# Kernel tuning notes

Measured on AMD Instinct MI355X. Metric: run time of the kernel, lower is better.

## Reference

```python
import jax, jax.numpy as jnp
import numpy as np

B, NU, NI, D, P, C = 32768, 200000, 200000, 512, 8, 512
DC = D // P  # cluster_dim = 64
TAU = 1.0


def setup_inputs() -> dict:
    key = jax.random.key(0)
    k = jax.random.split(key, 6)
    return {
        "user_emb": jax.random.normal(k[0], (NU, D), jnp.float32),
        "centroids": jax.random.normal(k[1], (P, C, DC), jnp.float32),
        "item_mu": jax.random.normal(k[2], (NI, D), jnp.float32),
        "item_logvar": jax.random.normal(k[3], (NI, D), jnp.float32) * 0.1,
        "user_id": jax.random.randint(k[4], (B,), 0, NU, jnp.int64 if jax.config.jax_enable_x64 else jnp.int32),
        "item_id": jax.random.randint(k[5], (B,), 0, NI, jnp.int64 if jax.config.jax_enable_x64 else jnp.int32),
    }


def _encode_user(user_emb, centroids, user_id, key):
    # gather + split into P partitions: [B, P, DC]
    u = user_emb[user_id].reshape(-1, P, DC)
    # squared L2 distance via expansion (avoids [B,P,C,DC] intermediate)
    u2 = jnp.sum(u * u, axis=-1)                      # [B, P]
    c2 = jnp.sum(centroids * centroids, axis=-1)      # [P, C]
    cross = jnp.einsum("bpd,pcd->bpc", u, centroids)  # [B, P, C]
    dist2 = jnp.maximum(u2[:, :, None] + c2[None, :, :] - 2.0 * cross, 0.0)
    neg_dist = -jnp.sqrt(dist2 + 1e-12)               # logits = -pairwise L2
    logits = jax.nn.softmax(neg_dist, axis=-1)        # [B, P, C]
    # gumbel-softmax, hard=True (straight-through)
    gu = jax.random.uniform(key, neg_dist.shape, jnp.float32, 1e-10, 1.0)
    g = -jnp.log(-jnp.log(gu))
    y_soft = jax.nn.softmax((neg_dist + g) / TAU, axis=-1)
    onehot = jax.nn.one_hot(jnp.argmax(y_soft, axis=-1), C, dtype=y_soft.dtype)
    y_hard = onehot + y_soft - jax.lax.stop_gradient(y_soft)
    # gather selected centroid per partition and concat -> [B, D]
    enc = jnp.einsum("bpc,pcd->bpd", y_hard, centroids).reshape(-1, D)
    return enc, logits


def _reparameterize(mu, logvar, key):
    std = jnp.exp(0.5 * logvar)
    eps = jax.random.normal(key, std.shape, std.dtype)
    return eps * std + mu


def reference(user_emb, centroids, item_mu, item_logvar, user_id, item_id):
    key = jax.random.key(42)
    kg, ke = jax.random.split(key)
    user_vecs, logits = _encode_user(user_emb, centroids, user_id, kg)
    item_vecs = _reparameterize(item_mu[item_id], item_logvar[item_id], ke)
    score = jnp.sum(user_vecs * item_vecs, axis=-1)  # [B]
    return score, logits
```

## Files before the change

### kernel.cpp

```cpp
#include <hip/hip_runtime.h>
#include <cstdint>
#include <cstddef>

#define B_TOT 32768
#define NPART 8
#define NCLUS 512
#define DCL   64
#define DTOT  512
#define BTILE 16
#define ROWB  272

typedef _Float16 half8 __attribute__((ext_vector_type(8)));
typedef float    f32x4 __attribute__((ext_vector_type(4)));

__host__ __device__ __forceinline__ void tf2x32(uint32_t k0, uint32_t k1,
    uint32_t x0, uint32_t x1, uint32_t& o0, uint32_t& o1)
{
  const uint32_t k2 = k0 ^ k1 ^ 0x1BD11BDAu;
#define TFR(r) { x0 += x1; x1 = (x1 << r) | (x1 >> (32 - r)); x1 ^= x0; }
  x0 += k0; x1 += k1;
  TFR(13) TFR(15) TFR(26) TFR(6)
  x0 += k1; x1 += k2 + 1u;
  TFR(17) TFR(29) TFR(16) TFR(24)
  x0 += k2; x1 += k0 + 2u;
  TFR(13) TFR(15) TFR(26) TFR(6)
  x0 += k0; x1 += k1 + 3u;
  TFR(17) TFR(29) TFR(16) TFR(24)
  x0 += k1; x1 += k2 + 4u;
  TFR(13) TFR(15) TFR(26) TFR(6)
  x0 += k2; x1 += k0 + 5u;
#undef TFR
  o0 = x0; o1 = x1;
}

__device__ __forceinline__ uint32_t tf_bits32(uint32_t k0, uint32_t k1, uint32_t n)
{
  uint32_t a, b;
  tf2x32(k0, k1, 0u, n, a, b);
  return a ^ b;
}

__device__ __forceinline__ float erfinv_xla(float x)
{
  float w = -log1pf(-x * x);
  float p;
  if (w < 5.0f) {
    w = w - 2.5f;
    p = 2.81022636e-08f;
    p = fmaf(p, w, 3.43273939e-07f);
    p = fmaf(p, w, -3.5233877e-06f);
    p = fmaf(p, w, -4.39150654e-06f);
    p = fmaf(p, w, 0.00021858087f);
    p = fmaf(p, w, -0.00125372503f);
    p = fmaf(p, w, -0.00417768164f);
    p = fmaf(p, w, 0.246640727f);
    p = fmaf(p, w, 1.50140941f);
  } else {
    w = __builtin_amdgcn_sqrtf(w) - 3.0f;
    p = -0.000200214257f;
    p = fmaf(p, w, 0.000100950558f);
    p = fmaf(p, w, 0.00134934322f);
    p = fmaf(p, w, -0.00367342844f);
    p = fmaf(p, w, 0.00573950773f);
    p = fmaf(p, w, -0.0076224613f);
    p = fmaf(p, w, 0.00943887047f);
    p = fmaf(p, w, 1.00167406f);
    p = fmaf(p, w, 2.83297682f);
  }
  return p * x;
}

__global__ __launch_bounds__(256) void qvae_prep_kernel(
    const float* __restrict__ centroids, _Float16* __restrict__ cimg)
{
  const int idx = blockIdx.x * 256 + threadIdx.x;
  const float* row = centroids + (size_t)idx * DCL;
  _Float16* orow = (_Float16*)((char*)cimg + (size_t)idx * ROWB);
  float s = 0.f;
#pragma unroll
  for (int d = 0; d < DCL; d += 4) {
    const float4 v = *(const float4*)(row + d);
    s = fmaf(v.x, v.x, s);
    s = fmaf(v.y, v.y, s);
    s = fmaf(v.z, v.z, s);
    s = fmaf(v.w, v.w, s);
  }
  *(float*)(orow + 128) = s;
#pragma unroll
  for (int d = 0; d < DCL; d += 8) {
    const float4 v0 = *(const float4*)(row + d);
    const float4 v1 = *(const float4*)(row + d + 4);
    const float vv[8] = { v0.x, v0.y, v0.z, v0.w, v1.x, v1.y, v1.z, v1.w };
    half8 hh, ll;
#pragma unroll
    for (int j = 0; j < 8; ++j) {
      const _Float16 h = (_Float16)vv[j];
      hh[j] = h;
      ll[j] = (_Float16)(vv[j] - (float)h);
    }
    *(half8*)(orow + d) = hh;
    *(half8*)(orow + 64 + d) = ll;
  }
}

__global__ __launch_bounds__(256, 4) void qvae_main_kernel(
    const float* __restrict__ user_emb, const _Float16* __restrict__ cimg,
    const int* __restrict__ user_id, float* __restrict__ out_logits,
    int* __restrict__ sel, uint32_t kg0, uint32_t kg1)
{
  __shared__ float u2s[BTILE];
  __shared__ float zZ[4][BTILE];
  __shared__ float zS[4][BTILE];
  __shared__ int   zA[4][BTILE];

  const int p = blockIdx.y;
  const int bbase = blockIdx.x * BTILE;
  const int tid = threadIdx.x;
  const int w  = tid >> 6;
  const int l  = tid & 63;
  const int lr = l & 15;
  const int q  = l >> 4;

  const int uid = user_id[bbase + lr];
  const float* urow = user_emb + (size_t)uid * DTOT + p * DCL;
  float uf[16];
  {
    const float4 a0 = *(const float4*)(urow + q * 8);
    const float4 a1 = *(const float4*)(urow + q * 8 + 4);
    const float4 a2 = *(const float4*)(urow + 32 + q * 8);
    const float4 a3 = *(const float4*)(urow + 32 + q * 8 + 4);
    uf[0]=a0.x;  uf[1]=a0.y;  uf[2]=a0.z;  uf[3]=a0.w;
    uf[4]=a1.x;  uf[5]=a1.y;  uf[6]=a1.z;  uf[7]=a1.w;
    uf[8]=a2.x;  uf[9]=a2.y;  uf[10]=a2.z; uf[11]=a2.w;
    uf[12]=a3.x; uf[13]=a3.y; uf[14]=a3.z; uf[15]=a3.w;
  }
  half8 ah[2], al[2];
#pragma unroll
  for (int m = 0; m < 2; ++m)
#pragma unroll
    for (int j = 0; j < 8; ++j) {
      const float v = uf[m * 8 + j];
      const _Float16 h = (_Float16)v;
      ah[m][j] = h;
      al[m][j] = (_Float16)(v - (float)h);
    }
  {
    float s = 0.f;
#pragma unroll
    for (int i = 0; i < 16; ++i) s = fmaf(uf[i], uf[i], s);
    s += __shfl_xor(s, 16);
    s += __shfl_xor(s, 32);
    if (tid < BTILE) u2s[tid] = s;
  }
  __syncthreads();
  float u2r[4];
  {
    const float4 uv = *(const float4*)&u2s[q * 4];
    u2r[0]=uv.x; u2r[1]=uv.y; u2r[2]=uv.z; u2r[3]=uv.w;
  }

  const int wcol = w * 32 + lr;
  const uint32_t nbw =
      ((uint32_t)(bbase + q * 4) * 8u + (uint32_t)p) * 512u + (uint32_t)wcol;
  const char* cb = (const char*)cimg;
  const uint32_t rowoff =
      ((uint32_t)p * NCLUS + (uint32_t)wcol) * (uint32_t)ROWB + (uint32_t)q * 16u;

  float ereg[32];
  float Zs[4]  = { 0.f, 0.f, 0.f, 0.f };
  float smx[4] = { -3.4e38f, -3.4e38f, -3.4e38f, -3.4e38f };
  int   sag[4] = { 0, 0, 0, 0 };

#define CDELT(i) ((((i) >> 1) * 128) + (((i) & 1) * 16))
#define BDELT(i) ((uint32_t)(CDELT(i)) * (uint32_t)ROWB)

#define LOADT(S, i)                                                           \
  {                                                                           \
    const uint32_t vo = rowoff + BDELT(i);                                    \
    bh0##S = *(const half8*)(cb + vo);                                        \
    bh1##S = *(const half8*)(cb + vo + 64);                                   \
    bl0##S = *(const half8*)(cb + vo + 128);                                  \
    bl1##S = *(const half8*)(cb + vo + 192);                                  \
    c2##S  = *(const float*)(cb + (vo - q * 16) + 256);                       \
  }

#define COMPT(S, i)                                                           \
  {                                                                           \
    f32x4 acc = { 0.f, 0.f, 0.f, 0.f };                                       \
    acc = __builtin_amdgcn_mfma_f32_16x16x32_f16(ah[0], bh0##S, acc, 0, 0, 0);\
    acc = __builtin_amdgcn_mfma_f32_16x16x32_f16(ah[1], bh1##S, acc, 0, 0, 0);\
    acc = __builtin_amdgcn_mfma_f32_16x16x32_f16(al[0], bh0##S, acc, 0, 0, 0);\
    acc = __builtin_amdgcn_mfma_f32_16x16x32_f16(al[1], bh1##S, acc, 0, 0, 0);\
    acc = __builtin_amdgcn_mfma_f32_16x16x32_f16(ah[0], bl0##S, acc, 0, 0, 0);\
    acc = __builtin_amdgcn_mfma_f32_16x16x32_f16(ah[1], bl1##S, acc, 0, 0, 0);\
    const uint32_t ncol = nbw + (uint32_t)CDELT(i);                           \
    const int colc = wcol + CDELT(i);                                         \
    _Pragma("unroll")                                                         \
    for (int r = 0; r < 4; ++r) {                                             \
      const float u2c2 = __fadd_rn(u2r[r], c2##S);                            \
      const float d2 = fmaxf(fmaf(-2.0f, acc[r], u2c2), 0.0f);                \
      const float qd = __builtin_amdgcn_sqrtf(__fadd_rn(d2, 1e-12f));         \
      const uint32_t bits = tf_bits32(kg0, kg1, ncol + (uint32_t)r * 4096u);  \
      const float u01 = __uint_as_float((bits >> 9) | 0x3f800000u) - 1.0f;    \
      const float gu = __fadd_rn(u01, 1e-10f);   \
      const float g = -__logf(-__logf(gu));                                   \
      const float sc = __fsub_rn(g, qd);                                      \
      if (sc > smx[r]) { smx[r] = sc; sag[r] = colc; }                        \
      const float e = __expf(-qd);                   \
      ereg[(i) * 4 + r] = e;                                                  \
      Zs[r] = __fadd_rn(Zs[r], e);                                            \
    }                                                                         \
  }

  half8 bh0A, bh1A, bl0A, bl1A; float c2A;
  half8 bh0B, bh1B, bl0B, bl1B; float c2B;
  LOADT(A, 0)
  LOADT(B, 1)
  COMPT(A, 0)
  LOADT(A, 2)
  COMPT(B, 1)
  LOADT(B, 3)
  COMPT(A, 2)
  LOADT(A, 4)
  COMPT(B, 3)
  LOADT(B, 5)
  COMPT(A, 4)
  LOADT(A, 6)
  COMPT(B, 5)
  LOADT(B, 7)
  COMPT(A, 6)
  COMPT(B, 7)

#pragma unroll
  for (int m = 1; m < 16; m <<= 1) {
#pragma unroll
    for (int r = 0; r < 4; ++r) {
      Zs[r] += __shfl_xor(Zs[r], m);
      const float os = __shfl_xor(smx[r], m);
      const int   oa = __shfl_xor(sag[r], m);
      if (os > smx[r] || (os == smx[r] && oa < sag[r])) { smx[r] = os; sag[r] = oa; }
    }
  }
  if (lr == 0) {
#pragma unroll
    for (int r = 0; r < 4; ++r) {
      zZ[w][q * 4 + r] = Zs[r];
      zS[w][q * 4 + r] = smx[r];
      zA[w][q * 4 + r] = sag[r];
    }
  }
  __syncthreads();

  float Zf[4]  = { 0.f, 0.f, 0.f, 0.f };
  float smf[4] = { -3.4e38f, -3.4e38f, -3.4e38f, -3.4e38f };
  int   saf[4] = { 0, 0, 0, 0 };
#pragma unroll
  for (int wv = 0; wv < 4; ++wv) {
    const float4 zz = *(const float4*)&zZ[wv][q * 4];
    const float4 ss = *(const float4*)&zS[wv][q * 4];
    const int4   aa = *(const int4*)&zA[wv][q * 4];
    const float zv[4] = { zz.x, zz.y, zz.z, zz.w };
    const float sv[4] = { ss.x, ss.y, ss.z, ss.w };
    const int   av[4] = { aa.x, aa.y, aa.z, aa.w };
#pragma unroll
    for (int r = 0; r < 4; ++r) {
      Zf[r] = __fadd_rn(Zf[r], zv[r]);
      if (sv[r] > smf[r] || (sv[r] == smf[r] && av[r] < saf[r])) {
        smf[r] = sv[r]; saf[r] = av[r];
      }
    }
  }

  float inv[4];
#pragma unroll
  for (int r = 0; r < 4; ++r) inv[r] = __builtin_amdgcn_rcpf(Zf[r]);

  float* obase = out_logits + ((size_t)(bbase + q * 4) * 8 + p) * 512 + wcol;
#pragma unroll
  for (int i = 0; i < 8; ++i)
#pragma unroll
    for (int r = 0; r < 4; ++r)
      obase[(size_t)r * 4096 + CDELT(i)] = ereg[i * 4 + r] * inv[r];

  if (w == 0 && lr == 0) {
#pragma unroll
    for (int r = 0; r < 4; ++r)
      sel[(bbase + q * 4 + r) * NPART + p] = saf[r];
  }
#undef CDELT
#undef BDELT
#undef LOADT
#undef COMPT
}

__global__ __launch_bounds__(256) void qvae_score_kernel(
    const float* __restrict__ centroids, const float* __restrict__ item_mu,
    const float* __restrict__ item_logvar, const int* __restrict__ item_id,
    const int* __restrict__ sel, float* __restrict__ out_score,
    uint32_t ke0, uint32_t ke1)
{
  const int lane = threadIdx.x & 63;
  const int b = blockIdx.x * 4 + (threadIdx.x >> 6);
  const int iid = item_id[b];
  const int pp = lane >> 3;
  const int sc = sel[b * NPART + pp];

  const float* cen = centroids + ((size_t)pp * NCLUS + sc) * DCL + (lane & 7) * 8;
  const float* mu = item_mu + (size_t)iid * DTOT + lane * 8;
  const float* lv = item_logvar + (size_t)iid * DTOT + lane * 8;

  const float4 m0 = *(const float4*)mu;
  const float4 m1 = *(const float4*)(mu + 4);
  const float4 l0 = *(const float4*)lv;
  const float4 l1 = *(const float4*)(lv + 4);
  const float4 q0 = *(const float4*)cen;
  const float4 q1 = *(const float4*)(cen + 4);
  const float mua[8] = { m0.x, m0.y, m0.z, m0.w, m1.x, m1.y, m1.z, m1.w };
  const float lva[8] = { l0.x, l0.y, l0.z, l0.w, l1.x, l1.y, l1.z, l1.w };
  const float cna[8] = { q0.x, q0.y, q0.z, q0.w, q1.x, q1.y, q1.z, q1.w };

  const float LO = __int_as_float(0xBF7FFFFFu);
  const float SQ2 = __int_as_float(0x3FB504F3u);
  const uint32_t nb = (uint32_t)b * 512u + (uint32_t)lane * 8u;

  float acc = 0.f;
#pragma unroll
  for (int k = 0; k < 8; ++k) {
    const uint32_t bits = tf_bits32(ke0, ke1, nb + (uint32_t)k);
    const float u01 = __uint_as_float((bits >> 9) | 0x3f800000u) - 1.0f;
    const float uu = fmaxf(LO, __fadd_rn(__fmul_rn(u01, 2.0f), LO));
    const float eps = __fmul_rn(SQ2, erfinv_xla(uu));
    const float sd = __expf(__fmul_rn(0.5f, lva[k]));
    const float it = __fadd_rn(__fmul_rn(eps, sd), mua[k]);
    acc = fmaf(cna[k], it, acc);
  }
#pragma unroll
  for (int m = 1; m < 64; m <<= 1) acc += __shfl_xor(acc, m);
  if (lane == 0) out_score[b] = acc;
}

extern "C" void kernel_launch(void* const* d_in, const int* in_sizes, int n_in,
                              void* d_out, int out_size, void* d_ws, size_t ws_size,
                              hipStream_t stream)
{
  (void)in_sizes; (void)n_in; (void)out_size; (void)ws_size;

  const float* user_emb    = (const float*)d_in[0];
  const float* centroids   = (const float*)d_in[1];
  const float* item_mu     = (const float*)d_in[2];
  const float* item_logvar = (const float*)d_in[3];
  const int*   user_id     = (const int*)d_in[4];
  const int*   item_id     = (const int*)d_in[5];

  float* out_score  = (float*)d_out;
  float* out_logits = (float*)d_out + B_TOT;

  int*       sel  = (int*)d_ws;
  _Float16*  cimg = (_Float16*)((char*)d_ws + (size_t)B_TOT * NPART * 4);

  uint32_t kg0, kg1, ke0, ke1;
  tf2x32(0u, 42u, 0u, 0u, kg0, kg1);
  tf2x32(0u, 42u, 0u, 1u, ke0, ke1);

  qvae_prep_kernel<<<NPART * NCLUS / 256, 256, 0, stream>>>(centroids, cimg);

  dim3 g1(B_TOT / BTILE, NPART);
  qvae_main_kernel<<<g1, 256, 0, stream>>>(user_emb, cimg, user_id,
                                           out_logits, sel, kg0, kg1);
  qvae_score_kernel<<<B_TOT / 4, 256, 0, stream>>>(centroids, item_mu, item_logvar,
                                                   item_id, sel, out_score, ke0, ke1);
}
```

Baseline: 483.1 us.

## Replace gumbel argmax log with ratio comparison and split MFMA accumulators

The gumbel argmax is rewritten algebraically. Maximizing g - qd with g = -log(t) is the same as minimizing t / exp(-qd), so the second log per element is removed and the exp value already computed for the softmax is reused. The comparison is done by cross-multiplication, which avoids a division. The MFMA chain is split into two independent accumulators to shorten the dependency chain. Exact tie-breaking may change because of rounding, and the reductions now carry one extra value each.

```diff
diff --git a/kernel.cpp b/kernel.cpp
--- a/kernel.cpp
+++ b/kernel.cpp
@@ -110,7 +110,8 @@
 {
   __shared__ float u2s[BTILE];
   __shared__ float zZ[4][BTILE];
-  __shared__ float zS[4][BTILE];
+  __shared__ float zT[4][BTILE];
+  __shared__ float zE[4][BTILE];
   __shared__ int   zA[4][BTILE];
 
   const int p = blockIdx.y;
@@ -165,11 +166,13 @@
   const char* cb = (const char*)cimg;
   const uint32_t rowoff =
       ((uint32_t)p * NCLUS + (uint32_t)wcol) * (uint32_t)ROWB + (uint32_t)q * 16u;
+  const uint32_t c2off = rowoff - (uint32_t)(q * 16) + 256u;
 
   float ereg[32];
-  float Zs[4]  = { 0.f, 0.f, 0.f, 0.f };
-  float smx[4] = { -3.4e38f, -3.4e38f, -3.4e38f, -3.4e38f };
-  int   sag[4] = { 0, 0, 0, 0 };
+  float Zs[4] = { 0.f, 0.f, 0.f, 0.f };
+  float tmin[4] = { 3.4e38f, 3.4e38f, 3.4e38f, 3.4e38f };
+  float emin[4] = { 1.0f, 1.0f, 1.0f, 1.0f };
+  int   amin[4] = { 0, 0, 0, 0 };
 
 #define CDELT(i) ((((i) >> 1) * 128) + (((i) & 1) * 16))
 #define BDELT(i) ((uint32_t)(CDELT(i)) * (uint32_t)ROWB)
@@ -181,32 +184,35 @@
     bh1##S = *(const half8*)(cb + vo + 64);                                   \
     bl0##S = *(const half8*)(cb + vo + 128);                                  \
     bl1##S = *(const half8*)(cb + vo + 192);                                  \
-    c2##S  = *(const float*)(cb + (vo - q * 16) + 256);                       \
+    c2##S  = *(const float*)(cb + c2off + BDELT(i));                          \
   }
 
 #define COMPT(S, i)                                                           \
   {                                                                           \
-    f32x4 acc = { 0.f, 0.f, 0.f, 0.f };                                       \
-    acc = __builtin_amdgcn_mfma_f32_16x16x32_f16(ah[0], bh0##S, acc, 0, 0, 0);\
-    acc = __builtin_amdgcn_mfma_f32_16x16x32_f16(ah[1], bh1##S, acc, 0, 0, 0);\
-    acc = __builtin_amdgcn_mfma_f32_16x16x32_f16(al[0], bh0##S, acc, 0, 0, 0);\
-    acc = __builtin_amdgcn_mfma_f32_16x16x32_f16(al[1], bh1##S, acc, 0, 0, 0);\
-    acc = __builtin_amdgcn_mfma_f32_16x16x32_f16(ah[0], bl0##S, acc, 0, 0, 0);\
-    acc = __builtin_amdgcn_mfma_f32_16x16x32_f16(ah[1], bl1##S, acc, 0, 0, 0);\
+    f32x4 accA = { 0.f, 0.f, 0.f, 0.f };                                      \
+    f32x4 accB = { 0.f, 0.f, 0.f, 0.f };                                      \
+    accA = __builtin_amdgcn_mfma_f32_16x16x32_f16(ah[0], bh0##S, accA, 0, 0, 0);\
+    accB = __builtin_amdgcn_mfma_f32_16x16x32_f16(ah[1], bh1##S, accB, 0, 0, 0);\
+    accA = __builtin_amdgcn_mfma_f32_16x16x32_f16(al[0], bh0##S, accA, 0, 0, 0);\
+    accB = __builtin_amdgcn_mfma_f32_16x16x32_f16(al[1], bh1##S, accB, 0, 0, 0);\
+    accA = __builtin_amdgcn_mfma_f32_16x16x32_f16(ah[0], bl0##S, accA, 0, 0, 0);\
+    accB = __builtin_amdgcn_mfma_f32_16x16x32_f16(ah[1], bl1##S, accB, 0, 0, 0);\
     const uint32_t ncol = nbw + (uint32_t)CDELT(i);                           \
-    const int colc = wcol + CDELT(i);                                         \
     _Pragma("unroll")                                                         \
     for (int r = 0; r < 4; ++r) {                                             \
       const float u2c2 = __fadd_rn(u2r[r], c2##S);                            \
-      const float d2 = fmaxf(fmaf(-2.0f, acc[r], u2c2), 0.0f);                \
+      const float d2 =                                                        \
+          fmaxf(fmaf(-2.0f, accA[r], fmaf(-2.0f, accB[r], u2c2)), 0.0f);      \
       const float qd = __builtin_amdgcn_sqrtf(__fadd_rn(d2, 1e-12f));         \
       const uint32_t bits = tf_bits32(kg0, kg1, ncol + (uint32_t)r * 4096u);  \
       const float u01 = __uint_as_float((bits >> 9) | 0x3f800000u) - 1.0f;    \
-      const float gu = __fadd_rn(u01, 1e-10f);   \
-      const float g = -__logf(-__logf(gu));                                   \
-      const float sc = __fsub_rn(g, qd);                                      \
-      if (sc > smx[r]) { smx[r] = sc; sag[r] = colc; }                        \
+      const float gu = __fadd_rn(u01, 1e-10f);            \
+      const float t = -__logf(gu);                  \
       const float e = __expf(-qd);                   \
+            \
+      if (__fmul_rn(t, emin[r]) < __fmul_rn(tmin[r], e)) {                    \
+        tmin[r] = t; emin[r] = e; amin[r] = (i);                              \
+      }                                                                       \
       ereg[(i) * 4 + r] = e;                                                  \
       Zs[r] = __fadd_rn(Zs[r], e);                                            \
     }                                                                         \
@@ -231,42 +237,58 @@
   COMPT(A, 6)
   COMPT(B, 7)
 
+  int colm[4];
+#pragma unroll
+  for (int r = 0; r < 4; ++r)
+    colm[r] = wcol + ((amin[r] >> 1) << 7) + ((amin[r] & 1) << 4);
+
 #pragma unroll
   for (int m = 1; m < 16; m <<= 1) {
 #pragma unroll
     for (int r = 0; r < 4; ++r) {
       Zs[r] += __shfl_xor(Zs[r], m);
-      const float os = __shfl_xor(smx[r], m);
-      const int   oa = __shfl_xor(sag[r], m);
-      if (os > smx[r] || (os == smx[r] && oa < sag[r])) { smx[r] = os; sag[r] = oa; }
+      const float ot = __shfl_xor(tmin[r], m);
+      const float oe = __shfl_xor(emin[r], m);
+      const int   oa = __shfl_xor(colm[r], m);
+      const float lhs = __fmul_rn(ot, emin[r]);
+      const float rhs = __fmul_rn(tmin[r], oe);
+      if (lhs < rhs || (lhs == rhs && oa < colm[r])) {
+        tmin[r] = ot; emin[r] = oe; colm[r] = oa;
+      }
     }
   }
   if (lr == 0) {
 #pragma unroll
     for (int r = 0; r < 4; ++r) {
       zZ[w][q * 4 + r] = Zs[r];
-      zS[w][q * 4 + r] = smx[r];
-      zA[w][q * 4 + r] = sag[r];
+      zT[w][q * 4 + r] = tmin[r];
+      zE[w][q * 4 + r] = emin[r];
+      zA[w][q * 4 + r] = colm[r];
     }
   }
   __syncthreads();
 
-  float Zf[4]  = { 0.f, 0.f, 0.f, 0.f };
-  float smf[4] = { -3.4e38f, -3.4e38f, -3.4e38f, -3.4e38f };
-  int   saf[4] = { 0, 0, 0, 0 };
+  float Zf[4] = { 0.f, 0.f, 0.f, 0.f };
+  float tf_[4] = { 3.4e38f, 3.4e38f, 3.4e38f, 3.4e38f };
+  float ef_[4] = { 1.0f, 1.0f, 1.0f, 1.0f };
+  int   af_[4] = { 0, 0, 0, 0 };
 #pragma unroll
   for (int wv = 0; wv < 4; ++wv) {
     const float4 zz = *(const float4*)&zZ[wv][q * 4];
-    const float4 ss = *(const float4*)&zS[wv][q * 4];
+    const float4 tt = *(const float4*)&zT[wv][q * 4];
+    const float4 ee = *(const float4*)&zE[wv][q * 4];
     const int4   aa = *(const int4*)&zA[wv][q * 4];
     const float zv[4] = { zz.x, zz.y, zz.z, zz.w };
-    const float sv[4] = { ss.x, ss.y, ss.z, ss.w };
+    const float tv[4] = { tt.x, tt.y, tt.z, tt.w };
+    const float ev[4] = { ee.x, ee.y, ee.z, ee.w };
     const int   av[4] = { aa.x, aa.y, aa.z, aa.w };
 #pragma unroll
     for (int r = 0; r < 4; ++r) {
       Zf[r] = __fadd_rn(Zf[r], zv[r]);
-      if (sv[r] > smf[r] || (sv[r] == smf[r] && av[r] < saf[r])) {
-        smf[r] = sv[r]; saf[r] = av[r];
+      const float lhs = __fmul_rn(tv[r], ef_[r]);
+      const float rhs = __fmul_rn(tf_[r], ev[r]);
+      if (lhs < rhs || (lhs == rhs && av[r] < af_[r])) {
+        tf_[r] = tv[r]; ef_[r] = ev[r]; af_[r] = av[r];
       }
     }
   }
@@ -285,7 +307,7 @@
   if (w == 0 && lr == 0) {
 #pragma unroll
     for (int r = 0; r < 4; ++r)
-      sel[(bbase + q * 4 + r) * NPART + p] = saf[r];
+      sel[(bbase + q * 4 + r) * NPART + p] = af_[r];
   }
 #undef CDELT
 #undef BDELT
```

After: 523.4 us. 1.08x slower.
